# Optimization experiments

Measured on AMD Instinct MI355X. Metric: run time of the kernel, lower is better.

## Reference

```python
import jax, jax.numpy as jnp
import numpy as np

N_NODES = 100000
D_IN = 128
D_HID = 256
N_EDGES = 3200000


def setup_inputs() -> dict:
    key = jax.random.key(0)
    k_x, k_e, k_w1, k_w2 = jax.random.split(key, 4)
    x = jax.random.normal(k_x, (N_NODES, D_IN), dtype=jnp.float32)
    edge_index = jax.random.randint(k_e, (2, N_EDGES), 0, N_NODES, dtype=jnp.int64)
    # Glorot-style init for GCN linear weights; PyG GCNConv has bias by default.
    W1 = jax.random.normal(k_w1, (D_IN, D_HID), dtype=jnp.float32) / np.sqrt(D_IN)
    b1 = jnp.zeros((D_HID,), dtype=jnp.float32)
    W2 = jax.random.normal(k_w2, (D_HID, D_HID), dtype=jnp.float32) / np.sqrt(D_HID)
    b2 = jnp.zeros((D_HID,), dtype=jnp.float32)
    return {"x": x, "edge_index": edge_index, "W1": W1, "b1": b1, "W2": W2, "b2": b2}


def gcn_conv(x, edge_index, W, b, num_nodes):
    # PyG GCNConv: add self-loops, symmetric normalization D^-1/2 A D^-1/2,
    # linear transform, scatter-add aggregation, bias.
    loop = jnp.arange(num_nodes, dtype=edge_index.dtype)
    src = jnp.concatenate([edge_index[0], loop])  # [E+N]
    dst = jnp.concatenate([edge_index[1], loop])  # [E+N]
    deg = jax.ops.segment_sum(jnp.ones_like(src, dtype=x.dtype), dst,
                              num_segments=num_nodes)  # in-degree incl. self-loop
    dinv = jnp.where(deg > 0, deg ** -0.5, 0.0)
    norm = dinv[src] * dinv[dst]  # [E+N]
    h = x @ W  # [N, D_out] -- transform before propagate (PyG order)
    msg = h[src] * norm[:, None]  # gather + scale: [E+N, D_out]
    out = jax.ops.segment_sum(msg, dst, num_segments=num_nodes)  # scatter-add
    return out + b


def reference(x, edge_index, W1, b1, W2, b2):
    n = x.shape[0]
    h = gcn_conv(x, edge_index, W1, b1, n)
    h = jax.nn.relu(h)
    # dropout is identity in eval mode (reference baseline runs deterministic)
    out = gcn_conv(h, edge_index, W2, b2, n)
    return out
```

## Files before the change

kernel.cpp:

```cpp
#include <hip/hip_runtime.h>


#define DF 256

typedef float f4v __attribute__((ext_vector_type(4)));
__device__ inline void nt_store4(float* p, float4 v) {
  f4v t;
  t.x = v.x; t.y = v.y; t.z = v.z; t.w = v.w;
  __builtin_nontemporal_store(t, (f4v*)p);
}
__device__ inline unsigned short f2bf(float f) {
  unsigned u = __float_as_uint(f);
  return (unsigned short)((u + 0x7FFFu + ((u >> 16) & 1u)) >> 16);
}
__device__ inline float bf2f(unsigned short h) {
  return __uint_as_float(((unsigned)h) << 16);
}

__global__ __launch_bounds__(256) void zero_i32(int* __restrict__ p, int n) {
  int i = blockIdx.x * blockDim.x + threadIdx.x;
  if (i < n) p[i] = 0;
}

__global__ __launch_bounds__(256) void detect_kernel(const int* __restrict__ ei32,
                                                     int n_logical,
                                                     int* __restrict__ flag) {
  __shared__ int s_nonzero;
  if (threadIdx.x == 0) s_nonzero = 0;
  __syncthreads();
  const int n_half = n_logical >> 1;
  int step = n_half / 1024;
  if (step < 1) step = 1;
  for (int k = threadIdx.x; k < 1024; k += 256) {
    long idx = (long)k * step;
    if (idx < n_half && ei32[2 * idx + 1] != 0) atomicOr(&s_nonzero, 1);
  }
  __syncthreads();
  if (threadIdx.x == 0) flag[0] = s_nonzero ? 0 : 1;
}

__global__ __launch_bounds__(256) void convert_kernel(const int* __restrict__ ei32,
                                                      const int* __restrict__ flag,
                                                      int* __restrict__ conv, int n) {
  int i = blockIdx.x * blockDim.x + threadIdx.x;
  if (i < n) conv[i] = flag[0] ? ei32[2 * (size_t)i] : ei32[i];
}

__global__ __launch_bounds__(256) void count_kernel(const int* __restrict__ dst,
                                                    int* __restrict__ cnt, int E, int n) {
  int i = blockIdx.x * blockDim.x + threadIdx.x;
  if (i < E) {
    int d = dst[i];
    if ((unsigned)d < (unsigned)n) atomicAdd(&cnt[d], 1);
  }
}

__global__ __launch_bounds__(1024) void scan_kernel(const int* __restrict__ cnt,
                                                    int* __restrict__ row_ptr, int n) {
  __shared__ int wsum[16];
  __shared__ int s_base;
  const int tid = threadIdx.x;
  const int lane = tid & 63;
  const int wid = tid >> 6;
  if (tid == 0) s_base = 0;
  __syncthreads();
  for (int start = 0; start < n; start += 4096) {
    const int i0 = start + tid * 4;
    int v[4];
#pragma unroll
    for (int u = 0; u < 4; ++u) v[u] = (i0 + u < n) ? cnt[i0 + u] : 0;
    const int tsum = v[0] + v[1] + v[2] + v[3];
    int sc = tsum;
#pragma unroll
    for (int off = 1; off < 64; off <<= 1) {
      int t = __shfl_up(sc, off);
      if (lane >= off) sc += t;
    }
    if (lane == 63) wsum[wid] = sc;
    __syncthreads();
    if (wid == 0) {
      int ws = (lane < 16) ? wsum[lane] : 0;
#pragma unroll
      for (int off = 1; off < 16; off <<= 1) {
        int t = __shfl_up(ws, off);
        if (lane >= off) ws += t;
      }
      if (lane < 16) wsum[lane] = ws;
    }
    __syncthreads();
    int base = s_base + (wid > 0 ? wsum[wid - 1] : 0) + (sc - tsum);
#pragma unroll
    for (int u = 0; u < 4; ++u) {
      if (i0 + u < n) row_ptr[i0 + u] = base;
      base += v[u];
    }
    __syncthreads();
    if (tid == 1023) s_base += wsum[15];
    __syncthreads();
  }
  if (tid == 0) row_ptr[n] = s_base;
}

__global__ __launch_bounds__(256) void dinv_cursor_kernel(const int* __restrict__ cnt,
                                                          const int* __restrict__ row_ptr,
                                                          float* __restrict__ dinv,
                                                          int* __restrict__ cursor, int n) {
  int i = blockIdx.x * blockDim.x + threadIdx.x;
  if (i < n) {
    dinv[i] = rsqrtf((float)(cnt[i] + 1));
    cursor[i] = row_ptr[i];
  }
}

__global__ __launch_bounds__(256) void fill_kernel(const int* __restrict__ src,
                                                   const int* __restrict__ dst,
                                                   const float* __restrict__ dinv,
                                                   int* __restrict__ cursor,
                                                   int2* __restrict__ edge, int E, int n) {
  int i = blockIdx.x * blockDim.x + threadIdx.x;
  if (i < E) {
    int s = src[i], d = dst[i];
    if ((unsigned)s < (unsigned)n && (unsigned)d < (unsigned)n) {
      int pos = atomicAdd(&cursor[d], 1);
      edge[pos] = make_int2(s, __float_as_int(dinv[s] * dinv[d]));
    }
  }
}

template <int K, bool RELU, bool OBF16>
__global__ __launch_bounds__(256) void gemm_kernel(const float* __restrict__ X,
                                                   const float* __restrict__ W,
                                                   const float* __restrict__ bias,
                                                   void* __restrict__ outv, int M) {
  __shared__ float xs[32][K];
  const int t = threadIdx.x;
  const int row0 = blockIdx.x * 32;

  for (int i = t; i < 8 * K; i += 256) {
    int r = i / (K / 4);
    int kk = (i % (K / 4)) * 4;
    int gr = row0 + r;
    float4 v = make_float4(0.f, 0.f, 0.f, 0.f);
    if (gr < M) v = *(const float4*)&X[(size_t)gr * K + kk];
    *(float4*)&xs[r][kk] = v;
  }
  __syncthreads();

  const int c = (t & 63) * 4;
  const int r0 = (t >> 6) * 8;
  float4 acc[8];
#pragma unroll
  for (int i = 0; i < 8; ++i) acc[i] = make_float4(0.f, 0.f, 0.f, 0.f);

  for (int k = 0; k < K; k += 4) {
    float4 wv[4];
#pragma unroll
    for (int j = 0; j < 4; ++j) wv[j] = *(const float4*)&W[(size_t)(k + j) * DF + c];
#pragma unroll
    for (int i = 0; i < 8; ++i) {
      float4 xv = *(const float4*)&xs[r0 + i][k];
      acc[i].x = fmaf(xv.x, wv[0].x, acc[i].x);
      acc[i].y = fmaf(xv.x, wv[0].y, acc[i].y);
      acc[i].z = fmaf(xv.x, wv[0].z, acc[i].z);
      acc[i].w = fmaf(xv.x, wv[0].w, acc[i].w);
      acc[i].x = fmaf(xv.y, wv[1].x, acc[i].x);
      acc[i].y = fmaf(xv.y, wv[1].y, acc[i].y);
      acc[i].z = fmaf(xv.y, wv[1].z, acc[i].z);
      acc[i].w = fmaf(xv.y, wv[1].w, acc[i].w);
      acc[i].x = fmaf(xv.z, wv[2].x, acc[i].x);
      acc[i].y = fmaf(xv.z, wv[2].y, acc[i].y);
      acc[i].z = fmaf(xv.z, wv[2].z, acc[i].z);
      acc[i].w = fmaf(xv.z, wv[2].w, acc[i].w);
      acc[i].x = fmaf(xv.w, wv[3].x, acc[i].x);
      acc[i].y = fmaf(xv.w, wv[3].y, acc[i].y);
      acc[i].z = fmaf(xv.w, wv[3].z, acc[i].z);
      acc[i].w = fmaf(xv.w, wv[3].w, acc[i].w);
    }
  }

  const float4 bv = *(const float4*)&bias[c];
#pragma unroll
  for (int i = 0; i < 8; ++i) {
    int gr = row0 + r0 + i;
    if (gr < M) {
      float4 r;
      r.x = acc[i].x + bv.x;
      r.y = acc[i].y + bv.y;
      r.z = acc[i].z + bv.z;
      r.w = acc[i].w + bv.w;
      if (RELU) {
        r.x = fmaxf(r.x, 0.f);
        r.y = fmaxf(r.y, 0.f);
        r.z = fmaxf(r.z, 0.f);
        r.w = fmaxf(r.w, 0.f);
      }
      if (OBF16) {
        ushort4 hq;
        hq.x = f2bf(r.x);
        hq.y = f2bf(r.y);
        hq.z = f2bf(r.z);
        hq.w = f2bf(r.w);
        *(ushort4*)&((unsigned short*)outv)[(size_t)gr * DF + c] = hq;
      } else {
        *(float4*)&((float*)outv)[(size_t)gr * DF + c] = r;
      }
    }
  }
}

__global__ __launch_bounds__(256) void agg256_kernel(const unsigned short* __restrict__ hb,
                                                     const int* __restrict__ row_ptr,
                                                     const int2* __restrict__ edge,
                                                     const float* __restrict__ dinv,
                                                     float* __restrict__ out, int n) {
  int wid = (blockIdx.x * blockDim.x + threadIdx.x) >> 6;
  int lane = threadIdx.x & 63;
  if (wid >= n) return;
  int start = row_ptr[wid];
  int end = row_ptr[wid + 1];
  const int foff = lane * 4;

  float4 acc = make_float4(0.f, 0.f, 0.f, 0.f);
  for (int base = start; base < end; base += 64) {
    int e = base + lane;
    int ce = 0;
    float we = 0.f;
    if (e < end) {
      long long ev = __builtin_nontemporal_load((const long long*)edge + e);
      ce = (int)(ev & 0xffffffffLL);
      we = __int_as_float((int)(ev >> 32));
    }
    int m = end - base;
    if (m > 64) m = 64;
    int j = 0;
    for (; j + 16 <= m; j += 16) {
      ushort4 hq[16];
      float ww[16];
#pragma unroll
      for (int u = 0; u < 16; ++u) {
        int s = __shfl(ce, j + u);
        ww[u] = __shfl(we, j + u);
        hq[u] = *(const ushort4*)&hb[(size_t)s * 256 + foff];
      }
#pragma unroll
      for (int u = 0; u < 16; ++u) {
        acc.x = fmaf(bf2f(hq[u].x), ww[u], acc.x);
        acc.y = fmaf(bf2f(hq[u].y), ww[u], acc.y);
        acc.z = fmaf(bf2f(hq[u].z), ww[u], acc.z);
        acc.w = fmaf(bf2f(hq[u].w), ww[u], acc.w);
      }
    }
    for (; j + 8 <= m; j += 8) {
      ushort4 hq[8];
      float ww[8];
#pragma unroll
      for (int u = 0; u < 8; ++u) {
        int s = __shfl(ce, j + u);
        ww[u] = __shfl(we, j + u);
        hq[u] = *(const ushort4*)&hb[(size_t)s * 256 + foff];
      }
#pragma unroll
      for (int u = 0; u < 8; ++u) {
        acc.x = fmaf(bf2f(hq[u].x), ww[u], acc.x);
        acc.y = fmaf(bf2f(hq[u].y), ww[u], acc.y);
        acc.z = fmaf(bf2f(hq[u].z), ww[u], acc.z);
        acc.w = fmaf(bf2f(hq[u].w), ww[u], acc.w);
      }
    }
    for (; j < m; ++j) {
      int s = __shfl(ce, j);
      float ww = __shfl(we, j);
      ushort4 hq = *(const ushort4*)&hb[(size_t)s * 256 + foff];
      acc.x = fmaf(bf2f(hq.x), ww, acc.x);
      acc.y = fmaf(bf2f(hq.y), ww, acc.y);
      acc.z = fmaf(bf2f(hq.z), ww, acc.z);
      acc.w = fmaf(bf2f(hq.w), ww, acc.w);
    }
  }
  float di = dinv[wid];
  float sw = di * di;
  ushort4 hq = *(const ushort4*)&hb[(size_t)wid * 256 + foff];
  acc.x = fmaf(bf2f(hq.x), sw, acc.x);
  acc.y = fmaf(bf2f(hq.y), sw, acc.y);
  acc.z = fmaf(bf2f(hq.z), sw, acc.z);
  acc.w = fmaf(bf2f(hq.w), sw, acc.w);
  nt_store4(&out[(size_t)wid * 256 + foff], acc);
}

__global__ __launch_bounds__(256) void agg128_kernel(const float* __restrict__ h,
                                                     const int* __restrict__ row_ptr,
                                                     const int2* __restrict__ edge,
                                                     const float* __restrict__ dinv,
                                                     float* __restrict__ out, int n) {
  int wid = (blockIdx.x * blockDim.x + threadIdx.x) >> 6;
  int lane = threadIdx.x & 63;
  if (wid >= n) return;
  int start = row_ptr[wid];
  int end = row_ptr[wid + 1];
  const int half = lane >> 5;
  const int foff = (lane & 31) * 4;

  float4 acc = make_float4(0.f, 0.f, 0.f, 0.f);
  for (int base = start; base < end; base += 64) {
    int e = base + lane;
    int ce = 0;
    float we = 0.f;
    if (e < end) {
      long long ev = __builtin_nontemporal_load((const long long*)edge + e);
      ce = (int)(ev & 0xffffffffLL);
      we = __int_as_float((int)(ev >> 32));
    }
    int m = end - base;
    if (m > 64) m = 64;
    int j = 0;
    for (; j + 32 <= m; j += 32) {
      float4 hv[16];
      float ww[16];
#pragma unroll
      for (int u = 0; u < 16; ++u) {
        int idx = j + 2 * u + half;
        int s = __shfl(ce, idx);
        ww[u] = __shfl(we, idx);
        hv[u] = *(const float4*)&h[(size_t)s * 128 + foff];
      }
#pragma unroll
      for (int u = 0; u < 16; ++u) {
        acc.x = fmaf(hv[u].x, ww[u], acc.x);
        acc.y = fmaf(hv[u].y, ww[u], acc.y);
        acc.z = fmaf(hv[u].z, ww[u], acc.z);
        acc.w = fmaf(hv[u].w, ww[u], acc.w);
      }
    }
    for (; j + 16 <= m; j += 16) {
      float4 hv[8];
      float ww[8];
#pragma unroll
      for (int u = 0; u < 8; ++u) {
        int idx = j + 2 * u + half;
        int s = __shfl(ce, idx);
        ww[u] = __shfl(we, idx);
        hv[u] = *(const float4*)&h[(size_t)s * 128 + foff];
      }
#pragma unroll
      for (int u = 0; u < 8; ++u) {
        acc.x = fmaf(hv[u].x, ww[u], acc.x);
        acc.y = fmaf(hv[u].y, ww[u], acc.y);
        acc.z = fmaf(hv[u].z, ww[u], acc.z);
        acc.w = fmaf(hv[u].w, ww[u], acc.w);
      }
    }
    for (; j + 2 <= m; j += 2) {
      int idx = j + half;
      int s = __shfl(ce, idx);
      float ww = __shfl(we, idx);
      float4 hv = *(const float4*)&h[(size_t)s * 128 + foff];
      acc.x = fmaf(hv.x, ww, acc.x);
      acc.y = fmaf(hv.y, ww, acc.y);
      acc.z = fmaf(hv.z, ww, acc.z);
      acc.w = fmaf(hv.w, ww, acc.w);
    }
    if (j < m) {
      int s = __shfl(ce, j);
      float ww = __shfl(we, j);
      if (half == 0) {
        float4 hv = *(const float4*)&h[(size_t)s * 128 + foff];
        acc.x = fmaf(hv.x, ww, acc.x);
        acc.y = fmaf(hv.y, ww, acc.y);
        acc.z = fmaf(hv.z, ww, acc.z);
        acc.w = fmaf(hv.w, ww, acc.w);
      }
    }
  }
  acc.x += __shfl_xor(acc.x, 32);
  acc.y += __shfl_xor(acc.y, 32);
  acc.z += __shfl_xor(acc.z, 32);
  acc.w += __shfl_xor(acc.w, 32);
  if (half == 0) {
    float di = dinv[wid];
    float sw = di * di;
    float4 own = *(const float4*)&h[(size_t)wid * 128 + foff];
    acc.x = fmaf(own.x, sw, acc.x);
    acc.y = fmaf(own.y, sw, acc.y);
    acc.z = fmaf(own.z, sw, acc.z);
    acc.w = fmaf(own.w, sw, acc.w);
    nt_store4(&out[(size_t)wid * 128 + foff], acc);
  }
}

extern "C" void kernel_launch(void* const* d_in, const int* in_sizes, int n_in,
                              void* d_out, int out_size, void* d_ws, size_t ws_size,
                              hipStream_t stream) {
  const float* x = (const float*)d_in[0];
  const int* ei = (const int*)d_in[1];
  const float* W1 = (const float*)d_in[2];
  const float* b1 = (const float*)d_in[3];
  const float* W2 = (const float*)d_in[4];
  const float* b2 = (const float*)d_in[5];

  const int N = in_sizes[0] / 128;
  const int NE2 = in_sizes[1];
  const int E = NE2 / 2;

  char* p = (char*)d_ws;
  auto carve = [&](size_t bytes) {
    void* q = (void*)p;
    p += (bytes + 255) & ~(size_t)255;
    return q;
  };
  int* flag = (int*)carve(4);
  int* cnt = (int*)carve((size_t)N * 4);
  int* row_ptr = (int*)carve((size_t)(N + 1) * 4);
  int* cursor = (int*)carve((size_t)N * 4);
  float* dinv = (float*)carve((size_t)N * 4);
  int2* edge = (int2*)carve((size_t)E * 8);
  float* buf = (float*)carve((size_t)N * DF * 4);
  int* conv = (int*)buf;
  const int* src = conv;
  const int* dst = conv + E;
  unsigned short* hb = (unsigned short*)d_out;

  detect_kernel<<<1, 256, 0, stream>>>(ei, NE2, flag);
  convert_kernel<<<(NE2 + 255) / 256, 256, 0, stream>>>(ei, flag, conv, NE2);

  zero_i32<<<(N + 255) / 256, 256, 0, stream>>>(cnt, N);
  count_kernel<<<(E + 255) / 256, 256, 0, stream>>>(dst, cnt, E, N);
  scan_kernel<<<1, 1024, 0, stream>>>(cnt, row_ptr, N);
  dinv_cursor_kernel<<<(N + 255) / 256, 256, 0, stream>>>(cnt, row_ptr, dinv, cursor, N);
  fill_kernel<<<(E + 255) / 256, 256, 0, stream>>>(src, dst, dinv, cursor, edge, E, N);

  const int agg_blocks = (N * 64 + 255) / 256;

  agg128_kernel<<<agg_blocks, 256, 0, stream>>>(x, row_ptr, edge, dinv, buf, N);
  gemm_kernel<128, true, true><<<(N + 31) / 32, 256, 0, stream>>>(buf, W1, b1, hb, N);

  agg256_kernel<<<agg_blocks, 256, 0, stream>>>(hb, row_ptr, edge, dinv, buf, N);
  gemm_kernel<256, false, false><<<(N + 31) / 32, 256, 0, stream>>>(buf, W2, b2, d_out, N);
}
```

Baseline: 1.184 ms.

## Use bf16 MFMA for dense GEMMs and gather bf16 node features in first aggregation

```diff
diff --git a/kernel.cpp b/kernel.cpp
--- a/kernel.cpp
+++ b/kernel.cpp
@@ -4,6 +4,9 @@
 #define DF 256
 
 typedef float f4v __attribute__((ext_vector_type(4)));
+typedef short bf16x8 __attribute__((ext_vector_type(8)));
+typedef float f32x4 __attribute__((ext_vector_type(4)));
+
 __device__ inline void nt_store4(float* p, float4 v) {
   f4v t;
   t.x = v.x; t.y = v.y; t.z = v.z; t.w = v.w;
@@ -46,6 +49,30 @@
   if (i < n) conv[i] = flag[0] ? ei32[2 * (size_t)i] : ei32[i];
 }
 
+__global__ __launch_bounds__(256) void xconv_kernel(const float* __restrict__ x,
+                                                    unsigned short* __restrict__ xb,
+                                                    int n8) {
+  int i = blockIdx.x * blockDim.x + threadIdx.x;
+  if (i < n8) {
+    const float4 v0 = *(const float4*)&x[(size_t)i * 8];
+    const float4 v1 = *(const float4*)&x[(size_t)i * 8 + 4];
+    unsigned p0 = f2bf(v0.x) | ((unsigned)f2bf(v0.y) << 16);
+    unsigned p1 = f2bf(v0.z) | ((unsigned)f2bf(v0.w) << 16);
+    unsigned p2 = f2bf(v1.x) | ((unsigned)f2bf(v1.y) << 16);
+    unsigned p3 = f2bf(v1.z) | ((unsigned)f2bf(v1.w) << 16);
+    *(uint4*)&xb[(size_t)i * 8] = make_uint4(p0, p1, p2, p3);
+  }
+}
+
+__global__ __launch_bounds__(256) void wconv_kernel(const float* __restrict__ W,
+                                                    unsigned short* __restrict__ Wt, int K) {
+  int idx = blockIdx.x * blockDim.x + threadIdx.x;
+  if (idx < K * 256) {
+    int k = idx / 256, c = idx % 256;
+    Wt[c * K + k] = f2bf(W[idx]);
+  }
+}
+
 __global__ __launch_bounds__(256) void count_kernel(const int* __restrict__ dst,
                                                     int* __restrict__ cnt, int E, int n) {
   int i = blockIdx.x * blockDim.x + threadIdx.x;
@@ -129,80 +156,81 @@
 
 template <int K, bool RELU, bool OBF16>
 __global__ __launch_bounds__(256) void gemm_kernel(const float* __restrict__ X,
-                                                   const float* __restrict__ W,
+                                                   const unsigned short* __restrict__ Wt,
                                                    const float* __restrict__ bias,
                                                    void* __restrict__ outv, int M) {
-  __shared__ float xs[32][K];
+  __shared__ unsigned short as_[32 * K];
   const int t = threadIdx.x;
   const int row0 = blockIdx.x * 32;
 
-  for (int i = t; i < 8 * K; i += 256) {
-    int r = i / (K / 4);
-    int kk = (i % (K / 4)) * 4;
+  for (int i = t; i < 4 * K; i += 256) {
+    int r = i / (K / 8);
+    int kk = (i % (K / 8)) * 8;
     int gr = row0 + r;
-    float4 v = make_float4(0.f, 0.f, 0.f, 0.f);
-    if (gr < M) v = *(const float4*)&X[(size_t)gr * K + kk];
-    *(float4*)&xs[r][kk] = v;
+    float4 v0 = make_float4(0.f, 0.f, 0.f, 0.f), v1 = v0;
+    if (gr < M) {
+      v0 = *(const float4*)&X[(size_t)gr * K + kk];
+      v1 = *(const float4*)&X[(size_t)gr * K + kk + 4];
+    }
+    unsigned p0 = f2bf(v0.x) | ((unsigned)f2bf(v0.y) << 16);
+    unsigned p1 = f2bf(v0.z) | ((unsigned)f2bf(v0.w) << 16);
+    unsigned p2 = f2bf(v1.x) | ((unsigned)f2bf(v1.y) << 16);
+    unsigned p3 = f2bf(v1.z) | ((unsigned)f2bf(v1.w) << 16);
+    unsigned byte = (unsigned)((r * K + kk) * 2) ^ ((unsigned)(r & 7) << 4);
+    *(uint4*)((char*)as_ + byte) = make_uint4(p0, p1, p2, p3);
   }
   __syncthreads();
 
-  const int c = (t & 63) * 4;
-  const int r0 = (t >> 6) * 8;
-  float4 acc[8];
-#pragma unroll
-  for (int i = 0; i < 8; ++i) acc[i] = make_float4(0.f, 0.f, 0.f, 0.f);
-
-  for (int k = 0; k < K; k += 4) {
-    float4 wv[4];
-#pragma unroll
-    for (int j = 0; j < 4; ++j) wv[j] = *(const float4*)&W[(size_t)(k + j) * DF + c];
-#pragma unroll
-    for (int i = 0; i < 8; ++i) {
-      float4 xv = *(const float4*)&xs[r0 + i][k];
-      acc[i].x = fmaf(xv.x, wv[0].x, acc[i].x);
-      acc[i].y = fmaf(xv.x, wv[0].y, acc[i].y);
-      acc[i].z = fmaf(xv.x, wv[0].z, acc[i].z);
-      acc[i].w = fmaf(xv.x, wv[0].w, acc[i].w);
-      acc[i].x = fmaf(xv.y, wv[1].x, acc[i].x);
-      acc[i].y = fmaf(xv.y, wv[1].y, acc[i].y);
-      acc[i].z = fmaf(xv.y, wv[1].z, acc[i].z);
-      acc[i].w = fmaf(xv.y, wv[1].w, acc[i].w);
-      acc[i].x = fmaf(xv.z, wv[2].x, acc[i].x);
-      acc[i].y = fmaf(xv.z, wv[2].y, acc[i].y);
-      acc[i].z = fmaf(xv.z, wv[2].z, acc[i].z);
-      acc[i].w = fmaf(xv.z, wv[2].w, acc[i].w);
-      acc[i].x = fmaf(xv.w, wv[3].x, acc[i].x);
-      acc[i].y = fmaf(xv.w, wv[3].y, acc[i].y);
-      acc[i].z = fmaf(xv.w, wv[3].z, acc[i].z);
-      acc[i].w = fmaf(xv.w, wv[3].w, acc[i].w);
-    }
-  }
-
-  const float4 bv = *(const float4*)&bias[c];
-#pragma unroll
-  for (int i = 0; i < 8; ++i) {
-    int gr = row0 + r0 + i;
-    if (gr < M) {
-      float4 r;
-      r.x = acc[i].x + bv.x;
-      r.y = acc[i].y + bv.y;
-      r.z = acc[i].z + bv.z;
-      r.w = acc[i].w + bv.w;
-      if (RELU) {
-        r.x = fmaxf(r.x, 0.f);
-        r.y = fmaxf(r.y, 0.f);
-        r.z = fmaxf(r.z, 0.f);
-        r.w = fmaxf(r.w, 0.f);
-      }
-      if (OBF16) {
-        ushort4 hq;
-        hq.x = f2bf(r.x);
-        hq.y = f2bf(r.y);
-        hq.z = f2bf(r.z);
-        hq.w = f2bf(r.w);
-        *(ushort4*)&((unsigned short*)outv)[(size_t)gr * DF + c] = hq;
-      } else {
-        *(float4*)&((float*)outv)[(size_t)gr * DF + c] = r;
+  const int l = t & 63;
+  const int wv = t >> 6;
+  const int lc = l & 15;
+  const int lk = (l >> 4) * 8;
+
+  f32x4 acc[2][4];
+#pragma unroll
+  for (int i = 0; i < 2; ++i)
+#pragma unroll
+    for (int j = 0; j < 4; ++j) acc[i][j] = (f32x4)0.f;
+
+#pragma unroll
+  for (int ks = 0; ks < K / 32; ++ks) {
+    bf16x8 a[2];
+#pragma unroll
+    for (int mrep = 0; mrep < 2; ++mrep) {
+      int row = mrep * 16 + lc;
+      unsigned byte = (unsigned)((row * K + ks * 32 + lk) * 2) ^ ((unsigned)(row & 7) << 4);
+      a[mrep] = *(const bf16x8*)((const char*)as_ + byte);
+    }
+    bf16x8 b[4];
+#pragma unroll
+    for (int nf = 0; nf < 4; ++nf) {
+      int col = wv * 64 + nf * 16 + lc;
+      b[nf] = *(const bf16x8*)&Wt[(size_t)col * K + ks * 32 + lk];
+    }
+#pragma unroll
+    for (int mrep = 0; mrep < 2; ++mrep)
+#pragma unroll
+      for (int nf = 0; nf < 4; ++nf)
+        acc[mrep][nf] = __builtin_amdgcn_mfma_f32_16x16x32_bf16(a[mrep], b[nf], acc[mrep][nf], 0, 0, 0);
+  }
+
+#pragma unroll
+  for (int nf = 0; nf < 4; ++nf) {
+    int gcol = wv * 64 + nf * 16 + lc;
+    float bv = bias[gcol];
+#pragma unroll
+    for (int mrep = 0; mrep < 2; ++mrep) {
+#pragma unroll
+      for (int r = 0; r < 4; ++r) {
+        int grow = row0 + mrep * 16 + (l >> 4) * 4 + r;
+        if (grow < M) {
+          float val = acc[mrep][nf][r] + bv;
+          if (RELU) val = fmaxf(val, 0.f);
+          if (OBF16)
+            ((unsigned short*)outv)[(size_t)grow * DF + gcol] = f2bf(val);
+          else
+            ((float*)outv)[(size_t)grow * DF + gcol] = val;
+        }
       }
     }
   }
@@ -287,7 +315,7 @@
   nt_store4(&out[(size_t)wid * 256 + foff], acc);
 }
 
-__global__ __launch_bounds__(256) void agg128_kernel(const float* __restrict__ h,
+__global__ __launch_bounds__(256) void agg128_kernel(const unsigned short* __restrict__ xb,
                                                      const int* __restrict__ row_ptr,
                                                      const int2* __restrict__ edge,
                                                      const float* __restrict__ dinv,
@@ -314,60 +342,42 @@
     if (m > 64) m = 64;
     int j = 0;
     for (; j + 32 <= m; j += 32) {
-      float4 hv[16];
+      ushort4 hq[16];
       float ww[16];
 #pragma unroll
       for (int u = 0; u < 16; ++u) {
         int idx = j + 2 * u + half;
         int s = __shfl(ce, idx);
         ww[u] = __shfl(we, idx);
-        hv[u] = *(const float4*)&h[(size_t)s * 128 + foff];
+        hq[u] = *(const ushort4*)&xb[(size_t)s * 128 + foff];
       }
 #pragma unroll
       for (int u = 0; u < 16; ++u) {
-        acc.x = fmaf(hv[u].x, ww[u], acc.x);
-        acc.y = fmaf(hv[u].y, ww[u], acc.y);
-        acc.z = fmaf(hv[u].z, ww[u], acc.z);
-        acc.w = fmaf(hv[u].w, ww[u], acc.w);
-      }
-    }
-    for (; j + 16 <= m; j += 16) {
-      float4 hv[8];
-      float ww[8];
-#pragma unroll
-      for (int u = 0; u < 8; ++u) {
-        int idx = j + 2 * u + half;
-        int s = __shfl(ce, idx);
-        ww[u] = __shfl(we, idx);
-        hv[u] = *(const float4*)&h[(size_t)s * 128 + foff];
-      }
-#pragma unroll
-      for (int u = 0; u < 8; ++u) {
-        acc.x = fmaf(hv[u].x, ww[u], acc.x);
-        acc.y = fmaf(hv[u].y, ww[u], acc.y);
-        acc.z = fmaf(hv[u].z, ww[u], acc.z);
-        acc.w = fmaf(hv[u].w, ww[u], acc.w);
+        acc.x = fmaf(bf2f(hq[u].x), ww[u], acc.x);
+        acc.y = fmaf(bf2f(hq[u].y), ww[u], acc.y);
+        acc.z = fmaf(bf2f(hq[u].z), ww[u], acc.z);
+        acc.w = fmaf(bf2f(hq[u].w), ww[u], acc.w);
       }
     }
     for (; j + 2 <= m; j += 2) {
       int idx = j + half;
       int s = __shfl(ce, idx);
       float ww = __shfl(we, idx);
-      float4 hv = *(const float4*)&h[(size_t)s * 128 + foff];
-      acc.x = fmaf(hv.x, ww, acc.x);
-      acc.y = fmaf(hv.y, ww, acc.y);
-      acc.z = fmaf(hv.z, ww, acc.z);
-      acc.w = fmaf(hv.w, ww, acc.w);
+      ushort4 hq = *(const ushort4*)&xb[(size_t)s * 128 + foff];
+      acc.x = fmaf(bf2f(hq.x), ww, acc.x);
+      acc.y = fmaf(bf2f(hq.y), ww, acc.y);
+      acc.z = fmaf(bf2f(hq.z), ww, acc.z);
+      acc.w = fmaf(bf2f(hq.w), ww, acc.w);
     }
     if (j < m) {
       int s = __shfl(ce, j);
       float ww = __shfl(we, j);
       if (half == 0) {
-        float4 hv = *(const float4*)&h[(size_t)s * 128 + foff];
-        acc.x = fmaf(hv.x, ww, acc.x);
-        acc.y = fmaf(hv.y, ww, acc.y);
-        acc.z = fmaf(hv.z, ww, acc.z);
-        acc.w = fmaf(hv.w, ww, acc.w);
+        ushort4 hq = *(const ushort4*)&xb[(size_t)s * 128 + foff];
+        acc.x = fmaf(bf2f(hq.x), ww, acc.x);
+        acc.y = fmaf(bf2f(hq.y), ww, acc.y);
+        acc.z = fmaf(bf2f(hq.z), ww, acc.z);
+        acc.w = fmaf(bf2f(hq.w), ww, acc.w);
       }
     }
   }
@@ -378,11 +388,11 @@
   if (half == 0) {
     float di = dinv[wid];
     float sw = di * di;
-    float4 own = *(const float4*)&h[(size_t)wid * 128 + foff];
-    acc.x = fmaf(own.x, sw, acc.x);
-    acc.y = fmaf(own.y, sw, acc.y);
-    acc.z = fmaf(own.z, sw, acc.z);
-    acc.w = fmaf(own.w, sw, acc.w);
+    ushort4 hq = *(const ushort4*)&xb[(size_t)wid * 128 + foff];
+    acc.x = fmaf(bf2f(hq.x), sw, acc.x);
+    acc.y = fmaf(bf2f(hq.y), sw, acc.y);
+    acc.z = fmaf(bf2f(hq.z), sw, acc.z);
+    acc.w = fmaf(bf2f(hq.w), sw, acc.w);
     nt_store4(&out[(size_t)wid * 128 + foff], acc);
   }
 }
@@ -413,14 +423,20 @@
   int* cursor = (int*)carve((size_t)N * 4);
   float* dinv = (float*)carve((size_t)N * 4);
   int2* edge = (int2*)carve((size_t)E * 8);
+  unsigned short* Wt1 = (unsigned short*)carve(128 * 256 * 2);
+  unsigned short* Wt2 = (unsigned short*)carve(256 * 256 * 2);
   float* buf = (float*)carve((size_t)N * DF * 4);
   int* conv = (int*)buf;
   const int* src = conv;
   const int* dst = conv + E;
   unsigned short* hb = (unsigned short*)d_out;
+  unsigned short* xb = (unsigned short*)((char*)d_out + (size_t)N * 256 * 2);
 
   detect_kernel<<<1, 256, 0, stream>>>(ei, NE2, flag);
   convert_kernel<<<(NE2 + 255) / 256, 256, 0, stream>>>(ei, flag, conv, NE2);
+  xconv_kernel<<<(N * 128 / 8 + 255) / 256, 256, 0, stream>>>(x, xb, N * 128 / 8);
+  wconv_kernel<<<(128 * 256 + 255) / 256, 256, 0, stream>>>(W1, Wt1, 128);
+  wconv_kernel<<<(256 * 256 + 255) / 256, 256, 0, stream>>>(W2, Wt2, 256);
 
   zero_i32<<<(N + 255) / 256, 256, 0, stream>>>(cnt, N);
   count_kernel<<<(E + 255) / 256, 256, 0, stream>>>(dst, cnt, E, N);
@@ -430,9 +446,9 @@
 
   const int agg_blocks = (N * 64 + 255) / 256;
 
-  agg128_kernel<<<agg_blocks, 256, 0, stream>>>(x, row_ptr, edge, dinv, buf, N);
-  gemm_kernel<128, true, true><<<(N + 31) / 32, 256, 0, stream>>>(buf, W1, b1, hb, N);
+  agg128_kernel<<<agg_blocks, 256, 0, stream>>>(xb, row_ptr, edge, dinv, buf, N);
+  gemm_kernel<128, true, true><<<(N + 31) / 32, 256, 0, stream>>>(buf, Wt1, b1, hb, N);
 
   agg256_kernel<<<agg_blocks, 256, 0, stream>>>(hb, row_ptr, edge, dinv, buf, N);
-  gemm_kernel<256, false, false><<<(N + 31) / 32, 256, 0, stream>>>(buf, W2, b2, d_out, N);
-}
+  gemm_kernel<256, false, false><<<(N + 31) / 32, 256, 0, stream>>>(buf, Wt2, b2, d_out, N);
+}
```

Result: faster. 999.5 us (-15.6%).
